# Optimization experiments

Hardware: AMD Instinct MI355X
Metric: run time of the kernel (lower is better)

## Reference

```python
import jax, jax.numpy as jnp
import numpy as np

N_QUBITS = 4
N_LAYERS = 2
ENT = [(i, (i + 1) % N_QUBITS) for i in range(N_QUBITS)]  # fixed entangling ring


def _ry(t):
    c, s = jnp.cos(t / 2), jnp.sin(t / 2)
    return jnp.stack([jnp.stack([c, -s]), jnp.stack([s, c])]).astype(jnp.complex64)


def _rx(t):
    c, s = jnp.cos(t / 2), jnp.sin(t / 2)
    return jnp.stack([jnp.stack([c + 0j, -1j * s]), jnp.stack([-1j * s, c + 0j])]).astype(jnp.complex64)


def _rz(t):
    e = jnp.exp(-0.5j * t.astype(jnp.complex64))
    z = jnp.zeros_like(e)
    return jnp.stack([jnp.stack([e, z]), jnp.stack([z, jnp.conj(e)])])


def _apply_1q(state, U, w):
    # state: (2,)*N_QUBITS; apply 2x2 U on wire w
    s = jnp.moveaxis(state, w, 0)
    s = jnp.tensordot(U, s, ((1,), (0,)))
    return jnp.moveaxis(s, 0, w)


def _cnot(state, c, t):
    s = jnp.moveaxis(state, (c, t), (0, 1))
    s = jnp.concatenate([s[:1], jnp.flip(s[1:], axis=1)], axis=0)
    return jnp.moveaxis(s, (0, 1), (c, t))


def _ansatz(state, vec, params):
    for i in range(N_QUBITS):
        state = _apply_1q(state, _ry(vec[i]), i)
    for l in range(N_LAYERS):
        for i in range(N_QUBITS):
            state = _apply_1q(state, _rx(params[l, i, 0]), i)
            state = _apply_1q(state, _ry(params[l, i, 1]), i)
            state = _apply_1q(state, _rz(params[l, i, 2]), i)
        for a_, b_ in ENT:
            state = _cnot(state, a_, b_)
    return state


def _adjoint_ansatz(state, vec, params):
    # inverse gates in reverse order
    for l in reversed(range(N_LAYERS)):
        for a_, b_ in reversed(ENT):
            state = _cnot(state, a_, b_)  # CNOT is self-inverse
        for i in reversed(range(N_QUBITS)):
            state = _apply_1q(state, _rz(-params[l, i, 2]), i)
            state = _apply_1q(state, _ry(-params[l, i, 1]), i)
            state = _apply_1q(state, _rx(-params[l, i, 0]), i)
    for i in reversed(range(N_QUBITS)):
        state = _apply_1q(state, _ry(-vec[i]), i)
    return state


def setup_inputs() -> dict:
    key = jax.random.key(0)
    k1, k2, k3 = jax.random.split(key, 3)
    a = jax.random.normal(k1, (1024, N_QUBITS), dtype=jnp.float32)
    b = jax.random.normal(k2, (1024, N_QUBITS), dtype=jnp.float32)
    params = jax.random.normal(k3, (N_LAYERS, N_QUBITS, 3), dtype=jnp.float32)
    return {"a": a, "b": b, "params": params}


def reference(a, b, params):
    def pair(x, y):
        psi = jnp.zeros((2,) * N_QUBITS, jnp.complex64).at[(0,) * N_QUBITS].set(1.0)
        psi = _ansatz(psi, x, params)
        psi = _adjoint_ansatz(psi, y, params)
        probs = jnp.abs(psi) ** 2
        # expval of PauliZ on wire 0: +1 for |0>, -1 for |1> on axis 0
        z = jnp.sum(probs[0]) - jnp.sum(probs[1])
        return jnp.abs(z)

    # Gram matrix [len(a), len(b)]
    return jax.vmap(lambda x: jax.vmap(lambda y: pair(x, y))(b))(a)
```

## Files before the change

kernel.cpp:

```cpp
#include <hip/hip_runtime.h>


#define NA 1024
#define NB 1024
#define KD 256
#define RT2 1.41421356237f

typedef __attribute__((ext_vector_type(8))) short bf16x8;
typedef __attribute__((ext_vector_type(4))) float f32x4;

__device__ __forceinline__ unsigned short f2bf(float x) {
    union { float f; unsigned u; } v; v.f = x;
    unsigned r = v.u + 0x7fffu + ((v.u >> 16) & 1u);
    return (unsigned short)(r >> 16);
}

__device__ __forceinline__ uint4 pack8(const float* f) {
    uint4 u;
    u.x = (unsigned)f2bf(f[0]) | ((unsigned)f2bf(f[1]) << 16);
    u.y = (unsigned)f2bf(f[2]) | ((unsigned)f2bf(f[3]) << 16);
    u.z = (unsigned)f2bf(f[4]) | ((unsigned)f2bf(f[5]) << 16);
    u.w = (unsigned)f2bf(f[6]) | ((unsigned)f2bf(f[7]) << 16);
    return u;
}

__device__ __forceinline__ void ry_gate(float* sr, float* si, int w, float t) {
    float s, c; __sincosf(0.5f * t, &s, &c);
    int st = 8 >> w;
    #pragma unroll
    for (int b = 0; b < 16; ++b) {
        if (b & st) continue;
        int j = b | st;
        float r0 = sr[b], i0 = si[b], r1 = sr[j], i1 = si[j];
        sr[b] = c * r0 - s * r1;  si[b] = c * i0 - s * i1;
        sr[j] = s * r0 + c * r1;  si[j] = s * i0 + c * i1;
    }
}

__device__ __forceinline__ void rx_gate(float* sr, float* si, int w, float t) {
    float s, c; __sincosf(0.5f * t, &s, &c);
    int st = 8 >> w;
    #pragma unroll
    for (int b = 0; b < 16; ++b) {
        if (b & st) continue;
        int j = b | st;
        float r0 = sr[b], i0 = si[b], r1 = sr[j], i1 = si[j];
        sr[b] = c * r0 + s * i1;  si[b] = c * i0 - s * r1;
        sr[j] = c * r1 + s * i0;  si[j] = c * i1 - s * r0;
    }
}

__device__ __forceinline__ void rz_gate(float* sr, float* si, int w, float t) {
    float s, c; __sincosf(0.5f * t, &s, &c);
    int st = 8 >> w;
    #pragma unroll
    for (int b = 0; b < 16; ++b) {
        if (b & st) continue;
        int j = b | st;
        float r0 = sr[b], i0 = si[b], r1 = sr[j], i1 = si[j];
        sr[b] = c * r0 + s * i0;  si[b] = c * i0 - s * r0;
        sr[j] = c * r1 - s * i1;  si[j] = c * i1 + s * r1;
    }
}

__device__ __forceinline__ void cnot_gate(float* sr, float* si, int cw, int tw) {
    int cs = 8 >> cw, ts = 8 >> tw;
    #pragma unroll
    for (int b = 0; b < 16; ++b) {
        if ((b & cs) && !(b & ts)) {
            int j = b | ts;
            float tr = sr[b]; sr[b] = sr[j]; sr[j] = tr;
            float ti = si[b]; si[b] = si[j]; si[j] = ti;
        }
    }
}

__device__ __forceinline__ void ansatz(float* sr, float* si, const float* vec, const float* P) {
    #pragma unroll
    for (int q = 0; q < 4; ++q) ry_gate(sr, si, q, vec[q]);
    #pragma unroll
    for (int l = 0; l < 2; ++l) {
        #pragma unroll
        for (int q = 0; q < 4; ++q) {
            rx_gate(sr, si, q, P[l * 12 + q * 3 + 0]);
            ry_gate(sr, si, q, P[l * 12 + q * 3 + 1]);
            rz_gate(sr, si, q, P[l * 12 + q * 3 + 2]);
        }
        cnot_gate(sr, si, 0, 1);
        cnot_gate(sr, si, 1, 2);
        cnot_gate(sr, si, 2, 3);
        cnot_gate(sr, si, 3, 0);
    }
}

__global__ __launch_bounds__(64) void qkm_phase1(
    const float* __restrict__ a, const float* __restrict__ b,
    const float* __restrict__ params,
    uint4* __restrict__ Qv, uint4* __restrict__ Mv) {
    float P[24];
    #pragma unroll
    for (int j = 0; j < 24; ++j) P[j] = params[j];
    int tid = threadIdx.x;
    int blk = blockIdx.x;

    if (blk < 128) {
        __shared__ float Wr[16][64];
        __shared__ float Wi[16][64];
        int g = tid >> 3, t = tid & 7;
        int y = (blk << 3) + g;
        float sr[16], si[16];
        #pragma unroll
        for (int k = 0; k < 16; ++k) { sr[k] = (k == 8 + t) ? 1.f : 0.f; si[k] = 0.f; }
        float vec[4];
        #pragma unroll
        for (int q = 0; q < 4; ++q) vec[q] = b[y * 4 + q];
        ansatz(sr, si, vec, P);
        #pragma unroll
        for (int l = 0; l < 16; ++l) { Wr[l][tid] = sr[l]; Wi[l][tid] = si[l]; }
        __syncthreads();
        int base = g << 3;
        #pragma unroll
        for (int kr = 0; kr < 2; ++kr) {
            int k = 2 * t + kr;
            float re[16], im[16];
            #pragma unroll
            for (int l = 0; l < 16; ++l) { re[l] = 0.f; im[l] = 0.f; }
            #pragma unroll
            for (int p2 = 0; p2 < 8; ++p2) {
                float wrk = Wr[k][base + p2], wik = Wi[k][base + p2];
                #pragma unroll
                for (int l = 0; l < 16; ++l) {
                    float wrl = Wr[l][base + p2], wil = Wi[l][base + p2];
                    re[l] += wrk * wrl + wik * wil;
                    im[l] += wil * wrk - wrl * wik;
                }
            }
            float row[16];
            #pragma unroll
            for (int l = 0; l < 16; ++l) {
                float off = (l < k) ? im[l] : re[l];
                row[l] = (l == k) ? (1.f - 2.f * re[l]) : (-2.f * RT2 * off);
            }
            uint4* d = Mv + y * 32 + k * 2;
            d[0] = pack8(row); d[1] = pack8(row + 8);
        }
    } else if (blk < 144) {
        int i = ((blk - 128) << 6) + tid;
        float sr[16], si[16];
        #pragma unroll
        for (int k = 0; k < 16; ++k) { sr[k] = (k == 0) ? 1.f : 0.f; si[k] = 0.f; }
        float vec[4];
        #pragma unroll
        for (int q = 0; q < 4; ++q) vec[q] = a[i * 4 + q];
        ansatz(sr, si, vec, P);
        #pragma unroll
        for (int k = 0; k < 16; ++k) {
            float rk = sr[k], ik = si[k];
            float row[16];
            #pragma unroll
            for (int l = 0; l < 16; ++l) {
                if (l < k)       row[l] = RT2 * (si[l] * rk - sr[l] * ik);
                else if (l == k) row[l] = rk * rk + ik * ik;
                else             row[l] = RT2 * (rk * sr[l] + ik * si[l]);
            }
            uint4* d = Qv + i * 32 + k * 2;
            d[0] = pack8(row); d[1] = pack8(row + 8);
        }
    }
}

__global__ __launch_bounds__(256) void qkm_phase2(
    const unsigned short* __restrict__ Q, const unsigned short* __restrict__ M,
    float* __restrict__ out) {
    int wave = threadIdx.x >> 6;
    int lane = threadIdx.x & 63;
    int blk = blockIdx.x;
    int xcd = blk & 7;
    int slot = blk >> 3;
    int bi = xcd * 2 + (slot >> 4);
    int bj = slot & 15;
    int wi = wave >> 1, wj = wave & 1;
    int row0 = bi * 64 + wi * 32;
    int col0 = bj * 64 + wj * 32;
    int m16 = lane & 15;
    int quad = lane >> 4;

    const unsigned short* q0 = Q + (size_t)(row0 + m16) * KD + quad * 8;
    const unsigned short* q1 = q0 + 16 * KD;
    const unsigned short* m0 = M + (size_t)(col0 + m16) * KD + quad * 8;
    const unsigned short* m1 = m0 + 16 * KD;

    f32x4 a00 = {0.f,0.f,0.f,0.f}, a01 = {0.f,0.f,0.f,0.f};
    f32x4 a10 = {0.f,0.f,0.f,0.f}, a11 = {0.f,0.f,0.f,0.f};
    #pragma unroll
    for (int kk = 0; kk < 8; ++kk) {
        bf16x8 qa = *(const bf16x8*)(q0 + kk * 32);
        bf16x8 qb = *(const bf16x8*)(q1 + kk * 32);
        bf16x8 ma = *(const bf16x8*)(m0 + kk * 32);
        bf16x8 mb = *(const bf16x8*)(m1 + kk * 32);
        a00 = __builtin_amdgcn_mfma_f32_16x16x32_bf16(qa, ma, a00, 0, 0, 0);
        a01 = __builtin_amdgcn_mfma_f32_16x16x32_bf16(qa, mb, a01, 0, 0, 0);
        a10 = __builtin_amdgcn_mfma_f32_16x16x32_bf16(qb, ma, a10, 0, 0, 0);
        a11 = __builtin_amdgcn_mfma_f32_16x16x32_bf16(qb, mb, a11, 0, 0, 0);
    }
    #pragma unroll
    for (int r = 0; r < 4; ++r) {
        int r0o = row0 + quad * 4 + r;
        int r1o = r0o + 16;
        out[r0o * NB + col0 + m16]      = fabsf(a00[r]);
        out[r0o * NB + col0 + 16 + m16] = fabsf(a01[r]);
        out[r1o * NB + col0 + m16]      = fabsf(a10[r]);
        out[r1o * NB + col0 + 16 + m16] = fabsf(a11[r]);
    }
}

extern "C" void kernel_launch(void* const* d_in, const int* in_sizes, int n_in,
                              void* d_out, int out_size, void* d_ws, size_t ws_size,
                              hipStream_t stream) {
    const float* a = (const float*)d_in[0];
    const float* b = (const float*)d_in[1];
    const float* params = (const float*)d_in[2];
    float* out = (float*)d_out;

    unsigned short* Q = (unsigned short*)d_ws;
    unsigned short* M = Q + (size_t)NA * KD;

    qkm_phase1<<<144, 64, 0, stream>>>(a, b, params, (uint4*)Q, (uint4*)M);
    qkm_phase2<<<256, 256, 0, stream>>>(Q, M, out);
}
```

Measured before the change: 70.40 us.

## Fuse state preparation and bf16 MFMA Gram product into one kernel

Merges the two kernels into a single launch. Each 64x64 output tile block recomputes the ansatz states for its 64 a-rows and 64 b-columns, builds the Q and M feature rows in registers, and stores them in swizzled LDS. MFMA then reads operands from LDS instead of a global workspace. This removes the second launch and the global round trip for Q and M, at the cost of redundant ansatz work (each b-row is recomputed by 16 blocks) and 78 KB of LDS per block, which limits occupancy.

```diff
diff --git a/kernel.cpp b/kernel.cpp
--- a/kernel.cpp
+++ b/kernel.cpp
@@ -3,7 +3,6 @@
 
 #define NA 1024
 #define NB 1024
-#define KD 256
 #define RT2 1.41421356237f
 
 typedef __attribute__((ext_vector_type(8))) short bf16x8;
@@ -93,124 +92,150 @@
     }
 }
 
-__global__ __launch_bounds__(64) void qkm_phase1(
+__global__ __launch_bounds__(512) void qkm_fused(
     const float* __restrict__ a, const float* __restrict__ b,
-    const float* __restrict__ params,
-    uint4* __restrict__ Qv, uint4* __restrict__ Mv) {
+    const float* __restrict__ params, float* __restrict__ out) {
+
+    __shared__ __align__(16) char LB[78336];
+    float* Wtr  = (float*)LB;
+    float* Wti  = Wtr + 8704;
+    float* Ptr_ = Wti + 8704;
+    float* Pti_ = Ptr_ + 1088;
+
+    const int tid = threadIdx.x;
+    const int blk = blockIdx.x;
+    const int xcd = blk & 7, slot = blk >> 3;
+    const int bi = xcd * 2 + (slot >> 4);
+    const int bj = slot & 15;
+    const int row0 = bi * 64, col0 = bj * 64;
+
     float P[24];
     #pragma unroll
     for (int j = 0; j < 24; ++j) P[j] = params[j];
-    int tid = threadIdx.x;
-    int blk = blockIdx.x;
-
-    if (blk < 128) {
-        __shared__ float Wr[16][64];
-        __shared__ float Wi[16][64];
-        int g = tid >> 3, t = tid & 7;
-        int y = (blk << 3) + g;
+
+    const int y  = tid >> 3;
+    const int k2 = tid & 7;
+
+    {
         float sr[16], si[16];
         #pragma unroll
-        for (int k = 0; k < 16; ++k) { sr[k] = (k == 8 + t) ? 1.f : 0.f; si[k] = 0.f; }
+        for (int k = 0; k < 16; ++k) { sr[k] = (k == 8 + k2) ? 1.f : 0.f; si[k] = 0.f; }
         float vec[4];
         #pragma unroll
-        for (int q = 0; q < 4; ++q) vec[q] = b[y * 4 + q];
+        for (int q = 0; q < 4; ++q) vec[q] = b[(col0 + y) * 4 + q];
         ansatz(sr, si, vec, P);
-        #pragma unroll
-        for (int l = 0; l < 16; ++l) { Wr[l][tid] = sr[l]; Wi[l][tid] = si[l]; }
-        __syncthreads();
-        int base = g << 3;
-        #pragma unroll
-        for (int kr = 0; kr < 2; ++kr) {
-            int k = 2 * t + kr;
-            float re[16], im[16];
-            #pragma unroll
-            for (int l = 0; l < 16; ++l) { re[l] = 0.f; im[l] = 0.f; }
-            #pragma unroll
-            for (int p2 = 0; p2 < 8; ++p2) {
-                float wrk = Wr[k][base + p2], wik = Wi[k][base + p2];
-                #pragma unroll
-                for (int l = 0; l < 16; ++l) {
-                    float wrl = Wr[l][base + p2], wil = Wi[l][base + p2];
-                    re[l] += wrk * wrl + wik * wil;
-                    im[l] += wil * wrk - wrl * wik;
-                }
-            }
-            float row[16];
-            #pragma unroll
-            for (int l = 0; l < 16; ++l) {
-                float off = (l < k) ? im[l] : re[l];
-                row[l] = (l == k) ? (1.f - 2.f * re[l]) : (-2.f * RT2 * off);
-            }
-            uint4* d = Mv + y * 32 + k * 2;
-            d[0] = pack8(row); d[1] = pack8(row + 8);
-        }
-    } else if (blk < 144) {
-        int i = ((blk - 128) << 6) + tid;
+        float* wr = Wtr + y * 136 + k2 * 17;
+        float* wi = Wti + y * 136 + k2 * 17;
+        #pragma unroll
+        for (int l = 0; l < 16; ++l) { wr[l] = sr[l]; wi[l] = si[l]; }
+    }
+    if (tid < 64) {
         float sr[16], si[16];
         #pragma unroll
         for (int k = 0; k < 16; ++k) { sr[k] = (k == 0) ? 1.f : 0.f; si[k] = 0.f; }
         float vec[4];
         #pragma unroll
-        for (int q = 0; q < 4; ++q) vec[q] = a[i * 4 + q];
+        for (int q = 0; q < 4; ++q) vec[q] = a[(row0 + tid) * 4 + q];
         ansatz(sr, si, vec, P);
-        #pragma unroll
-        for (int k = 0; k < 16; ++k) {
-            float rk = sr[k], ik = si[k];
-            float row[16];
-            #pragma unroll
-            for (int l = 0; l < 16; ++l) {
-                if (l < k)       row[l] = RT2 * (si[l] * rk - sr[l] * ik);
-                else if (l == k) row[l] = rk * rk + ik * ik;
-                else             row[l] = RT2 * (rk * sr[l] + ik * si[l]);
-            }
-            uint4* d = Qv + i * 32 + k * 2;
-            d[0] = pack8(row); d[1] = pack8(row + 8);
+        float* qr = Ptr_ + tid * 17;
+        float* qi = Pti_ + tid * 17;
+        #pragma unroll
+        for (int l = 0; l < 16; ++l) { qr[l] = sr[l]; qi[l] = si[l]; }
+    }
+    __syncthreads();
+
+    const int k0 = k2 * 2, k1 = k0 + 1;
+    float re0[16], im0[16], re1[16], im1[16];
+    #pragma unroll
+    for (int l = 0; l < 16; ++l) { re0[l] = 0.f; im0[l] = 0.f; re1[l] = 0.f; im1[l] = 0.f; }
+    const float* wyr = Wtr + y * 136;
+    const float* wyi = Wti + y * 136;
+    #pragma unroll
+    for (int p2 = 0; p2 < 8; ++p2) {
+        const float* br  = wyr + p2 * 17;
+        const float* bi_ = wyi + p2 * 17;
+        float ar0 = br[k0], ai0 = bi_[k0];
+        float ar1 = br[k1], ai1 = bi_[k1];
+        #pragma unroll
+        for (int l = 0; l < 16; ++l) {
+            float xr = br[l], xi = bi_[l];
+            re0[l] += ar0 * xr + ai0 * xi;
+            im0[l] += xi * ar0 - xr * ai0;
+            re1[l] += ar1 * xr + ai1 * xi;
+            im1[l] += xi * ar1 - xr * ai1;
         }
     }
-}
-
-__global__ __launch_bounds__(256) void qkm_phase2(
-    const unsigned short* __restrict__ Q, const unsigned short* __restrict__ M,
-    float* __restrict__ out) {
-    int wave = threadIdx.x >> 6;
-    int lane = threadIdx.x & 63;
-    int blk = blockIdx.x;
-    int xcd = blk & 7;
-    int slot = blk >> 3;
-    int bi = xcd * 2 + (slot >> 4);
-    int bj = slot & 15;
-    int wi = wave >> 1, wj = wave & 1;
-    int row0 = bi * 64 + wi * 32;
-    int col0 = bj * 64 + wj * 32;
-    int m16 = lane & 15;
-    int quad = lane >> 4;
-
-    const unsigned short* q0 = Q + (size_t)(row0 + m16) * KD + quad * 8;
-    const unsigned short* q1 = q0 + 16 * KD;
-    const unsigned short* m0 = M + (size_t)(col0 + m16) * KD + quad * 8;
-    const unsigned short* m1 = m0 + 16 * KD;
-
-    f32x4 a00 = {0.f,0.f,0.f,0.f}, a01 = {0.f,0.f,0.f,0.f};
-    f32x4 a10 = {0.f,0.f,0.f,0.f}, a11 = {0.f,0.f,0.f,0.f};
+    float rowm0[16], rowm1[16];
+    #pragma unroll
+    for (int l = 0; l < 16; ++l) {
+        float off0 = (l < k0) ? im0[l] : re0[l];
+        rowm0[l] = (l == k0) ? (1.f - 2.f * re0[l]) : (-2.f * RT2 * off0);
+        float off1 = (l < k1) ? im1[l] : re1[l];
+        rowm1[l] = (l == k1) ? (1.f - 2.f * re1[l]) : (-2.f * RT2 * off1);
+    }
+    uint4 m00 = pack8(rowm0), m01 = pack8(rowm0 + 8);
+    uint4 m10 = pack8(rowm1), m11 = pack8(rowm1 + 8);
+
+    const float* pr = Ptr_ + y * 17;
+    const float* pi = Pti_ + y * 17;
+    float rk0 = pr[k0], ik0 = pi[k0], rk1 = pr[k1], ik1 = pi[k1];
+    float rowq0[16], rowq1[16];
+    #pragma unroll
+    for (int l = 0; l < 16; ++l) {
+        float xr = pr[l], xi = pi[l];
+        rowq0[l] = (l < k0)  ? RT2 * (xi * rk0 - xr * ik0)
+                 : (l == k0) ? (rk0 * rk0 + ik0 * ik0)
+                 :             RT2 * (rk0 * xr + ik0 * xi);
+        rowq1[l] = (l < k1)  ? RT2 * (xi * rk1 - xr * ik1)
+                 : (l == k1) ? (rk1 * rk1 + ik1 * ik1)
+                 :             RT2 * (rk1 * xr + ik1 * xi);
+    }
+    uint4 q00 = pack8(rowq0), q01 = pack8(rowq0 + 8);
+    uint4 q10 = pack8(rowq1), q11 = pack8(rowq1 + 8);
+
+    __syncthreads();
+
+    char* Qsb = LB;
+    char* Msb = LB + 32768;
+    {
+        const int sy = (y & 15) << 4;
+        *(uint4*)(Msb + y * 512 + ((k0 * 32)      ^ sy)) = m00;
+        *(uint4*)(Msb + y * 512 + ((k0 * 32 + 16) ^ sy)) = m01;
+        *(uint4*)(Msb + y * 512 + ((k1 * 32)      ^ sy)) = m10;
+        *(uint4*)(Msb + y * 512 + ((k1 * 32 + 16) ^ sy)) = m11;
+        *(uint4*)(Qsb + y * 512 + ((k0 * 32)      ^ sy)) = q00;
+        *(uint4*)(Qsb + y * 512 + ((k0 * 32 + 16) ^ sy)) = q01;
+        *(uint4*)(Qsb + y * 512 + ((k1 * 32)      ^ sy)) = q10;
+        *(uint4*)(Qsb + y * 512 + ((k1 * 32 + 16) ^ sy)) = q11;
+    }
+    __syncthreads();
+
+    const int wave = tid >> 6, lane = tid & 63;
+    const int wi = wave >> 2, wj = wave & 3;
+    const int m16 = lane & 15, quad = lane >> 4;
+    const int rA0 = wi * 32 + m16;
+    const int rA1 = rA0 + 16;
+    const int rB  = wj * 16 + m16;
+    const int sA  = m16 << 4;
+    const char* qp0 = Qsb + rA0 * 512;
+    const char* qp1 = Qsb + rA1 * 512;
+    const char* mp  = Msb + rB  * 512;
+    f32x4 a0 = {0.f, 0.f, 0.f, 0.f}, a1 = {0.f, 0.f, 0.f, 0.f};
     #pragma unroll
     for (int kk = 0; kk < 8; ++kk) {
-        bf16x8 qa = *(const bf16x8*)(q0 + kk * 32);
-        bf16x8 qb = *(const bf16x8*)(q1 + kk * 32);
-        bf16x8 ma = *(const bf16x8*)(m0 + kk * 32);
-        bf16x8 mb = *(const bf16x8*)(m1 + kk * 32);
-        a00 = __builtin_amdgcn_mfma_f32_16x16x32_bf16(qa, ma, a00, 0, 0, 0);
-        a01 = __builtin_amdgcn_mfma_f32_16x16x32_bf16(qa, mb, a01, 0, 0, 0);
-        a10 = __builtin_amdgcn_mfma_f32_16x16x32_bf16(qb, ma, a10, 0, 0, 0);
-        a11 = __builtin_amdgcn_mfma_f32_16x16x32_bf16(qb, mb, a11, 0, 0, 0);
+        int cb = (kk * 64 + quad * 16) ^ sA;
+        bf16x8 qa = *(const bf16x8*)(qp0 + cb);
+        bf16x8 qb = *(const bf16x8*)(qp1 + cb);
+        bf16x8 ma = *(const bf16x8*)(mp  + cb);
+        a0 = __builtin_amdgcn_mfma_f32_16x16x32_bf16(qa, ma, a0, 0, 0, 0);
+        a1 = __builtin_amdgcn_mfma_f32_16x16x32_bf16(qb, ma, a1, 0, 0, 0);
     }
     #pragma unroll
     for (int r = 0; r < 4; ++r) {
-        int r0o = row0 + quad * 4 + r;
-        int r1o = r0o + 16;
-        out[r0o * NB + col0 + m16]      = fabsf(a00[r]);
-        out[r0o * NB + col0 + 16 + m16] = fabsf(a01[r]);
-        out[r1o * NB + col0 + m16]      = fabsf(a10[r]);
-        out[r1o * NB + col0 + 16 + m16] = fabsf(a11[r]);
+        int orow = row0 + wi * 32 + quad * 4 + r;
+        int ocol = col0 + wj * 16 + m16;
+        out[orow * NB + ocol]        = fabsf(a0[r]);
+        out[(orow + 16) * NB + ocol] = fabsf(a1[r]);
     }
 }
 
@@ -222,9 +247,6 @@
     const float* params = (const float*)d_in[2];
     float* out = (float*)d_out;
 
-    unsigned short* Q = (unsigned short*)d_ws;
-    unsigned short* M = Q + (size_t)NA * KD;
-
-    qkm_phase1<<<144, 64, 0, stream>>>(a, b, params, (uint4*)Q, (uint4*)M);
-    qkm_phase2<<<256, 256, 0, stream>>>(Q, M, out);
-}
+    (void)d_ws; (void)ws_size;
+    qkm_fused<<<256, 512, 0, stream>>>(a, b, params, out);
+}
```

Result: slower. 129.5 us (+84.0%).

## Restructure phase1 into 512-thread blocks with padded shared layout

Applied to the files above, without the earlier changes.

Phase1 moves from 144 blocks of 64 threads to 34 blocks of 512 threads. Each M block now simulates 32 b-vectors with 256 threads, then has all 512 threads build one row each from a padded (stride 17/136) shared-memory layout. The padding is meant to avoid bank conflicts, and the reorganisation doubles the threads working on the outer-product stage. The cost is far fewer blocks, so fewer CUs are busy, and half the threads sit idle during the ansatz stage.

```diff
diff --git a/kernel.cpp b/kernel.cpp
--- a/kernel.cpp
+++ b/kernel.cpp
@@ -93,59 +93,66 @@
     }
 }
 
-__global__ __launch_bounds__(64) void qkm_phase1(
+__global__ __launch_bounds__(512, 2) void qkm_phase1(
     const float* __restrict__ a, const float* __restrict__ b,
     const float* __restrict__ params,
     uint4* __restrict__ Qv, uint4* __restrict__ Mv) {
+
     float P[24];
     #pragma unroll
     for (int j = 0; j < 24; ++j) P[j] = params[j];
-    int tid = threadIdx.x;
-    int blk = blockIdx.x;
-
-    if (blk < 128) {
-        __shared__ float Wr[16][64];
-        __shared__ float Wi[16][64];
-        int g = tid >> 3, t = tid & 7;
-        int y = (blk << 3) + g;
-        float sr[16], si[16];
-        #pragma unroll
-        for (int k = 0; k < 16; ++k) { sr[k] = (k == 8 + t) ? 1.f : 0.f; si[k] = 0.f; }
-        float vec[4];
-        #pragma unroll
-        for (int q = 0; q < 4; ++q) vec[q] = b[y * 4 + q];
-        ansatz(sr, si, vec, P);
-        #pragma unroll
-        for (int l = 0; l < 16; ++l) { Wr[l][tid] = sr[l]; Wi[l][tid] = si[l]; }
+    const int tid = threadIdx.x;
+    const int blk = blockIdx.x;
+
+    if (blk < 32) {
+        __shared__ float Wtr[32 * 136];
+        __shared__ float Wti[32 * 136];
+        const int col0 = blk << 5;
+
+        if (tid < 256) {
+            const int y = tid >> 3, p2 = tid & 7;
+            float sr[16], si[16];
+            #pragma unroll
+            for (int k = 0; k < 16; ++k) { sr[k] = (k == 8 + p2) ? 1.f : 0.f; si[k] = 0.f; }
+            float vec[4];
+            #pragma unroll
+            for (int q = 0; q < 4; ++q) vec[q] = b[(col0 + y) * 4 + q];
+            ansatz(sr, si, vec, P);
+            float* wr = Wtr + y * 136 + p2 * 17;
+            float* wi = Wti + y * 136 + p2 * 17;
+            #pragma unroll
+            for (int l = 0; l < 16; ++l) { wr[l] = sr[l]; wi[l] = si[l]; }
+        }
         __syncthreads();
-        int base = g << 3;
-        #pragma unroll
-        for (int kr = 0; kr < 2; ++kr) {
-            int k = 2 * t + kr;
-            float re[16], im[16];
-            #pragma unroll
-            for (int l = 0; l < 16; ++l) { re[l] = 0.f; im[l] = 0.f; }
-            #pragma unroll
-            for (int p2 = 0; p2 < 8; ++p2) {
-                float wrk = Wr[k][base + p2], wik = Wi[k][base + p2];
-                #pragma unroll
-                for (int l = 0; l < 16; ++l) {
-                    float wrl = Wr[l][base + p2], wil = Wi[l][base + p2];
-                    re[l] += wrk * wrl + wik * wil;
-                    im[l] += wil * wrk - wrl * wik;
-                }
+
+        const int y = tid >> 4, k = tid & 15;
+        const float* wyr = Wtr + y * 136;
+        const float* wyi = Wti + y * 136;
+        float re[16], im[16];
+        #pragma unroll
+        for (int l = 0; l < 16; ++l) { re[l] = 0.f; im[l] = 0.f; }
+        #pragma unroll
+        for (int p2 = 0; p2 < 8; ++p2) {
+            const float* br  = wyr + p2 * 17;
+            const float* bi_ = wyi + p2 * 17;
+            float ar = br[k], ai = bi_[k];
+            #pragma unroll
+            for (int l = 0; l < 16; ++l) {
+                float xr = br[l], xi = bi_[l];
+                re[l] += ar * xr + ai * xi;
+                im[l] += xi * ar - xr * ai;
             }
-            float row[16];
-            #pragma unroll
-            for (int l = 0; l < 16; ++l) {
-                float off = (l < k) ? im[l] : re[l];
-                row[l] = (l == k) ? (1.f - 2.f * re[l]) : (-2.f * RT2 * off);
-            }
-            uint4* d = Mv + y * 32 + k * 2;
-            d[0] = pack8(row); d[1] = pack8(row + 8);
-        }
-    } else if (blk < 144) {
-        int i = ((blk - 128) << 6) + tid;
+        }
+        float row[16];
+        #pragma unroll
+        for (int l = 0; l < 16; ++l) {
+            float off = (l < k) ? im[l] : re[l];
+            row[l] = (l == k) ? (1.f - 2.f * re[l]) : (-2.f * RT2 * off);
+        }
+        uint4* d = Mv + (size_t)(col0 + y) * 32 + k * 2;
+        d[0] = pack8(row); d[1] = pack8(row + 8);
+    } else {
+        const int i = ((blk - 32) << 9) + tid;
         float sr[16], si[16];
         #pragma unroll
         for (int k = 0; k < 16; ++k) { sr[k] = (k == 0) ? 1.f : 0.f; si[k] = 0.f; }
@@ -163,7 +170,7 @@
                 else if (l == k) row[l] = rk * rk + ik * ik;
                 else             row[l] = RT2 * (rk * sr[l] + ik * si[l]);
             }
-            uint4* d = Qv + i * 32 + k * 2;
+            uint4* d = Qv + (size_t)i * 32 + k * 2;
             d[0] = pack8(row); d[1] = pack8(row + 8);
         }
     }
@@ -225,6 +232,6 @@
     unsigned short* Q = (unsigned short*)d_ws;
     unsigned short* M = Q + (size_t)NA * KD;
 
-    qkm_phase1<<<144, 64, 0, stream>>>(a, b, params, (uint4*)Q, (uint4*)M);
+    qkm_phase1<<<34, 512, 0, stream>>>(a, b, params, (uint4*)Q, (uint4*)M);
     qkm_phase2<<<256, 256, 0, stream>>>(Q, M, out);
 }
```

New measurement: 75.69 us. 1.08x slower.
